# Kernel tuning notes

Hardware: AMD Instinct MI355X
Metric: run time of the kernel (lower is better)

Reference implementation:

```python
import jax, jax.numpy as jnp
import numpy as np

B, T, C, H = 4, 2048, 2048, 16
HD = C // H  # head_size = 128
EPS = 1e-5


def layernorm(x, g, b):
    mu = jnp.mean(x, axis=-1, keepdims=True)
    var = jnp.var(x, axis=-1, keepdims=True)
    return (x - mu) * jax.lax.rsqrt(var + EPS) * g + b


def setup_inputs() -> dict:
    key = jax.random.key(0)
    ks = jax.random.split(key, 12)
    s_attn = 1.0 / np.sqrt(C)
    s_ffn1 = 1.0 / np.sqrt(C)
    s_ffn2 = 1.0 / np.sqrt(4 * C)
    return {
        "x": jax.random.normal(ks[0], (B, T, C), jnp.float32),
        "Wq": jax.random.normal(ks[1], (H, C, HD), jnp.float32) * s_attn,
        "Wk": jax.random.normal(ks[2], (H, C, HD), jnp.float32) * s_attn,
        "Wv": jax.random.normal(ks[3], (H, C, HD), jnp.float32) * s_attn,
        "Wp": jax.random.normal(ks[4], (C, C), jnp.float32) * s_attn,
        "bp": jnp.zeros((C,), jnp.float32),
        "W1": jax.random.normal(ks[5], (C, 4 * C), jnp.float32) * s_ffn1,
        "b1": jnp.zeros((4 * C,), jnp.float32),
        "W2": jax.random.normal(ks[6], (4 * C, C), jnp.float32) * s_ffn2,
        "b2": jnp.zeros((C,), jnp.float32),
        "g1": jnp.ones((C,), jnp.float32),
        "beta1": jnp.zeros((C,), jnp.float32),
        "g2": jnp.ones((C,), jnp.float32),
        "beta2": jnp.zeros((C,), jnp.float32),
    }


def reference(x, Wq, Wk, Wv, Wp, bp, W1, b1, W2, b2, g1, beta1, g2, beta2):
    # --- attention sublayer (pre-LN, causal) ---
    h = layernorm(x, g1, beta1)
    q = jnp.einsum("btc,hcd->bhtd", h, Wq)
    k = jnp.einsum("bsc,hcd->bhsd", h, Wk)
    v = jnp.einsum("bsc,hcd->bhsd", h, Wv)
    scores = jnp.einsum("bhtd,bhsd->bhts", q, k) / jnp.sqrt(jnp.asarray(HD, x.dtype))
    causal = jnp.tril(jnp.ones((T, T), bool))
    scores = jnp.where(causal, scores, jnp.asarray(-jnp.inf, x.dtype))
    w = jax.nn.softmax(scores, axis=-1)  # dropout = identity (eval mode)
    o = jnp.einsum("bhts,bhsd->bhtd", w, v)
    o = o.transpose(0, 2, 1, 3).reshape(B, T, C)  # concat heads
    x = x + o @ Wp + bp
    # --- feed-forward sublayer ---
    h2 = layernorm(x, g2, beta2)
    f = jax.nn.gelu(h2 @ W1 + b1, approximate=False)
    x = x + f @ W2 + b2
    return x
```

## Files before the change

### kernel.cpp

```cpp
#include <hip/hip_runtime.h>
#include <math.h>

#define B_ 4
#define T_ 2048
#define C_ 2048
#define H_ 16
#define HD_ 128

typedef __attribute__((ext_vector_type(8))) short short8;
typedef __attribute__((ext_vector_type(4))) float f32x4;
typedef unsigned short u16;

__device__ __forceinline__ u16 f2bf(float f) {
  union { float f; unsigned u; } v; v.f = f;
  unsigned r = v.u + 0x7FFFu + ((v.u >> 16) & 1u);
  return (u16)(r >> 16);
}

__device__ __forceinline__ void gld16(const void* g, void* l) {
  __builtin_amdgcn_global_load_lds(
      (__attribute__((address_space(1))) void*)(void*)g,
      (__attribute__((address_space(3))) void*)l, 16, 0, 0);
}

__global__ __launch_bounds__(256) void tconv(const float* __restrict__ in,
                                             u16* __restrict__ out,
                                             int K, int N,
                                             long inBS, long outBS) {
  __shared__ float tile[32][33];
  const float* inb = in + (long)blockIdx.z * inBS;
  u16* outb = out + (long)blockIdx.z * outBS;
  int k0 = blockIdx.x << 5, n0 = blockIdx.y << 5;
  int t = threadIdx.x;
  {
    int kk = t >> 3, nn = (t & 7) << 2;
    float4 v = *(const float4*)(inb + (long)(k0 + kk) * N + n0 + nn);
    tile[kk][nn + 0] = v.x; tile[kk][nn + 1] = v.y;
    tile[kk][nn + 2] = v.z; tile[kk][nn + 3] = v.w;
  }
  __syncthreads();
  {
    int nn = t >> 3, kk = (t & 7) << 2;
    ushort4 o;
    o.x = f2bf(tile[kk + 0][nn]); o.y = f2bf(tile[kk + 1][nn]);
    o.z = f2bf(tile[kk + 2][nn]); o.w = f2bf(tile[kk + 3][nn]);
    *(ushort4*)(outb + (long)(n0 + nn) * K + k0 + kk) = o;
  }
}

__global__ __launch_bounds__(256) void ln_rows(const float* __restrict__ x,
                                               const float* __restrict__ gam,
                                               const float* __restrict__ bet,
                                               u16* __restrict__ out) {
  int row = blockIdx.x;
  const float* xr = x + (size_t)row * C_;
  int t = threadIdx.x;
  float4 v0 = *(const float4*)(xr + t * 8);
  float4 v1 = *(const float4*)(xr + t * 8 + 4);
  float s = v0.x + v0.y + v0.z + v0.w + v1.x + v1.y + v1.z + v1.w;
  float ss = v0.x * v0.x + v0.y * v0.y + v0.z * v0.z + v0.w * v0.w +
             v1.x * v1.x + v1.y * v1.y + v1.z * v1.z + v1.w * v1.w;
  for (int d = 32; d > 0; d >>= 1) {
    s += __shfl_down(s, d);
    ss += __shfl_down(ss, d);
  }
  __shared__ float red[8];
  int wv = t >> 6;
  if ((t & 63) == 0) { red[wv] = s; red[4 + wv] = ss; }
  __syncthreads();
  s = red[0] + red[1] + red[2] + red[3];
  ss = red[4] + red[5] + red[6] + red[7];
  float mu = s * (1.0f / C_);
  float var = ss * (1.0f / C_) - mu * mu;
  float rs = rsqrtf(var + 1e-5f);
  int c = t * 8;
  float vv[8] = {v0.x, v0.y, v0.z, v0.w, v1.x, v1.y, v1.z, v1.w};
  ushort4 o0, o1;
  o0.x = f2bf((vv[0] - mu) * rs * gam[c + 0] + bet[c + 0]);
  o0.y = f2bf((vv[1] - mu) * rs * gam[c + 1] + bet[c + 1]);
  o0.z = f2bf((vv[2] - mu) * rs * gam[c + 2] + bet[c + 2]);
  o0.w = f2bf((vv[3] - mu) * rs * gam[c + 3] + bet[c + 3]);
  o1.x = f2bf((vv[4] - mu) * rs * gam[c + 4] + bet[c + 4]);
  o1.y = f2bf((vv[5] - mu) * rs * gam[c + 5] + bet[c + 5]);
  o1.z = f2bf((vv[6] - mu) * rs * gam[c + 6] + bet[c + 6]);
  o1.w = f2bf((vv[7] - mu) * rs * gam[c + 7] + bet[c + 7]);
  *(ushort4*)(out + (size_t)row * C_ + c) = o0;
  *(ushort4*)(out + (size_t)row * C_ + c + 4) = o1;
}

template <int EPI>
__global__ __launch_bounds__(512, 2) void gemm256(
    const u16* __restrict__ A, const u16* __restrict__ BT,
    int M, int N, int K, int lda, int ldb,
    u16* __restrict__ oq, u16* __restrict__ ok, u16* __restrict__ ovt,
    float* __restrict__ of32, const float* __restrict__ resid,
    const float* __restrict__ bias, u16* __restrict__ obf, int addBias) {
  extern __shared__ char smem[];
  int nbx = N >> 8;
  int nwg = gridDim.x;
  int flat = blockIdx.x;
  int sw = (flat & 7) * (nwg >> 3) + (flat >> 3);
  int bx = sw % nbx, by = sw / nbx;
  int m0 = by << 8, n0 = bx << 8;
  int tid = threadIdx.x;
  int lane = tid & 63, wave = tid >> 6;
  int wm = wave >> 2, wn = wave & 3;
  int l15 = lane & 15, l16 = lane >> 4;
  int nt = K >> 6;

  f32x4 acc[8][4] = {};
  short8 af[4][2], bf[4][2];

  auto stage = [&](int b, int r, int k0) {
    int row = (r & 3) * 64 + (tid >> 3);
    int lslot = (tid & 7) ^ (row & 7);
    char* dst = smem + ((r < 4) ? 0 : 65536) + b * 32768 + (r & 3) * 8192 + tid * 16;
    const u16* src = ((r < 4) ? (A + (long)(m0 + row) * lda)
                              : (BT + (long)(n0 + row) * ldb)) +
                     k0 + lslot * 8;
    gld16(src, dst);
  };
  auto ldA = [&](int cur, int mf, int kk) {
    int row = wm * 128 + mf * 16 + l15;
    int slot = (kk * 4 + l16) ^ (row & 7);
    return *(const short8*)(smem + cur * 32768 + row * 128 + slot * 16);
  };
  auto ldB = [&](int cur, int nf, int kk) {
    int row = wn * 64 + nf * 16 + l15;
    int slot = (kk * 4 + l16) ^ (row & 7);
    return *(const short8*)(smem + 65536 + cur * 32768 + row * 128 + slot * 16);
  };

#pragma unroll
  for (int r = 0; r < 8; ++r) stage(0, r, 0);

  for (int t = 0; t < nt; ++t) {
    int cur = t & 1, nxt = cur ^ 1;
    bool more = (t + 1) < nt;
    int k1 = (t + 1) << 6;
    if (more) {
      stage(nxt, 0, k1); stage(nxt, 1, k1); stage(nxt, 2, k1);
      asm volatile("s_waitcnt vmcnt(3)" ::: "memory");
    } else {
      asm volatile("s_waitcnt vmcnt(0)" ::: "memory");
    }
    __builtin_amdgcn_s_barrier();
#pragma unroll
    for (int mq = 0; mq < 4; ++mq)
#pragma unroll
      for (int kk = 0; kk < 2; ++kk) af[mq][kk] = ldA(cur, mq, kk);
#pragma unroll
    for (int nq = 0; nq < 2; ++nq)
#pragma unroll
      for (int kk = 0; kk < 2; ++kk) bf[nq][kk] = ldB(cur, nq, kk);
    if (more) { stage(nxt, 3, k1); stage(nxt, 4, k1); stage(nxt, 5, k1); }
    __builtin_amdgcn_s_barrier();
    asm volatile("s_waitcnt lgkmcnt(0)" ::: "memory");
    __builtin_amdgcn_s_setprio(1);
#pragma unroll
    for (int mq = 0; mq < 4; ++mq)
#pragma unroll
      for (int nq = 0; nq < 2; ++nq)
#pragma unroll
        for (int kk = 0; kk < 2; ++kk)
          acc[mq][nq] = __builtin_amdgcn_mfma_f32_16x16x32_bf16(
              af[mq][kk], bf[nq][kk], acc[mq][nq], 0, 0, 0);
    __builtin_amdgcn_s_setprio(0);
    __builtin_amdgcn_s_barrier();
#pragma unroll
    for (int nq = 2; nq < 4; ++nq)
#pragma unroll
      for (int kk = 0; kk < 2; ++kk) bf[nq][kk] = ldB(cur, nq, kk);
    if (more) { stage(nxt, 6, k1); stage(nxt, 7, k1); }
    __builtin_amdgcn_s_barrier();
    asm volatile("s_waitcnt lgkmcnt(0)" ::: "memory");
    __builtin_amdgcn_s_setprio(1);
#pragma unroll
    for (int mq = 0; mq < 4; ++mq)
#pragma unroll
      for (int nq = 2; nq < 4; ++nq)
#pragma unroll
        for (int kk = 0; kk < 2; ++kk)
          acc[mq][nq] = __builtin_amdgcn_mfma_f32_16x16x32_bf16(
              af[mq][kk], bf[nq][kk], acc[mq][nq], 0, 0, 0);
    __builtin_amdgcn_s_setprio(0);
    __builtin_amdgcn_s_barrier();
#pragma unroll
    for (int mq = 0; mq < 4; ++mq)
#pragma unroll
      for (int kk = 0; kk < 2; ++kk) af[mq][kk] = ldA(cur, 4 + mq, kk);
    __builtin_amdgcn_s_barrier();
    asm volatile("s_waitcnt lgkmcnt(0)" ::: "memory");
    __builtin_amdgcn_s_setprio(1);
#pragma unroll
    for (int mq = 0; mq < 4; ++mq)
#pragma unroll
      for (int nq = 0; nq < 2; ++nq)
#pragma unroll
        for (int kk = 0; kk < 2; ++kk)
          acc[4 + mq][nq] = __builtin_amdgcn_mfma_f32_16x16x32_bf16(
              af[mq][kk], bf[nq][kk], acc[4 + mq][nq], 0, 0, 0);
    __builtin_amdgcn_s_setprio(0);
    __builtin_amdgcn_s_barrier();
    __builtin_amdgcn_s_setprio(1);
#pragma unroll
    for (int mq = 0; mq < 4; ++mq)
#pragma unroll
      for (int nq = 2; nq < 4; ++nq)
#pragma unroll
        for (int kk = 0; kk < 2; ++kk)
          acc[4 + mq][nq] = __builtin_amdgcn_mfma_f32_16x16x32_bf16(
              af[mq][kk], bf[nq][kk], acc[4 + mq][nq], 0, 0, 0);
    __builtin_amdgcn_s_setprio(0);
    __builtin_amdgcn_s_barrier();
  }

#pragma unroll
  for (int mf = 0; mf < 8; ++mf) {
#pragma unroll
    for (int nf = 0; nf < 4; ++nf) {
      int rowf = m0 + wm * 128 + mf * 16 + l16 * 4;
      int col = n0 + wn * 64 + nf * 16 + l15;
      if constexpr (EPI == 0) {
        int seg = col >> 11, cn = col & 2047;
        int hh = cn >> 7, dd = cn & 127;
        int bb = rowf >> 11, t0 = rowf & 2047;
        if (seg == 2) {
          ushort4 o;
          o.x = f2bf(acc[mf][nf][0]); o.y = f2bf(acc[mf][nf][1]);
          o.z = f2bf(acc[mf][nf][2]); o.w = f2bf(acc[mf][nf][3]);
          *(ushort4*)(ovt + ((long)(bb * H_ + hh) * HD_ + dd) * T_ + t0) = o;
        } else {
          u16* dst = (seg == 0) ? oq : ok;
#pragma unroll
          for (int r = 0; r < 4; ++r)
            dst[((long)(bb * H_ + hh) * T_ + t0 + r) * HD_ + dd] =
                f2bf(acc[mf][nf][r]);
        }
      } else if constexpr (EPI == 1) {
#pragma unroll
        for (int r = 0; r < 4; ++r) {
          long idx = (long)(rowf + r) * N + col;
          of32[idx] = resid[idx] + bias[col] + acc[mf][nf][r];
        }
      } else if constexpr (EPI == 2) {
#pragma unroll
        for (int r = 0; r < 4; ++r) {
          float v = acc[mf][nf][r] + bias[col];
          float g = 0.5f * v * (1.0f + erff(v * 0.70710678118654752f));
          obf[(long)(rowf + r) * N + col] = f2bf(g);
        }
      } else {
#pragma unroll
        for (int r = 0; r < 4; ++r) {
          long idx = (long)(rowf + r) * N + col;
          float v = acc[mf][nf][r];
          if (addBias) v += bias[col];
          of32[idx] += v;
        }
      }
    }
  }
}

__global__ __launch_bounds__(256) void attn_fwd(const u16* __restrict__ q,
                                                const u16* __restrict__ k,
                                                const u16* __restrict__ vt,
                                                u16* __restrict__ o) {
  __shared__ u16 Ks[64 * 128];
  __shared__ u16 Vs[128 * 64];
  __shared__ u16 Ps[4][32 * 64];
  int bid = blockIdx.x;
  int bh = bid & 63;
  int qb = 15 - (bid >> 6);
  int q0 = qb << 7;
  int tid = threadIdx.x, lane = tid & 63, wave = tid >> 6;
  int l15 = lane & 15, l16 = lane >> 4;
  int wq0 = q0 + wave * 32;

  short8 qf[2][4];
#pragma unroll
  for (int rf = 0; rf < 2; ++rf)
#pragma unroll
    for (int kk = 0; kk < 4; ++kk)
      qf[rf][kk] = *(const short8*)(q + ((long)bh * T_ + wq0 + rf * 16 + l15) * HD_ +
                                    kk * 32 + l16 * 8);

  f32x4 accO[2][8] = {};
  float m_r[2][4], l_r[2][4];
#pragma unroll
  for (int rf = 0; rf < 2; ++rf)
#pragma unroll
    for (int r = 0; r < 4; ++r) { m_r[rf][r] = -INFINITY; l_r[rf][r] = 0.f; }
  const float sc = 0.08838834764831845f * 1.4426950408889634f;

  int nt = (q0 >> 6) + 2;
  int off0 = wave * 4096 + lane * 16;

  int4 kreg[4], vreg[4];
  auto regload = [&](int t) {
    int s0 = t << 6;
#pragma unroll
    for (int it = 0; it < 4; ++it) {
      int off = off0 + it * 1024;
      int krow = off >> 8;
      kreg[it] = *(const int4*)((const char*)(k + ((long)bh * T_ + s0 + krow) * HD_) +
                                (off & 255));
      int dd = off >> 7;
      vreg[it] = *(const int4*)((const char*)(vt + ((long)bh * HD_ + dd) * T_ + s0) +
                                (off & 127));
    }
  };
  auto dswrite = [&]() {
#pragma unroll
    for (int it = 0; it < 4; ++it) {
      int off = off0 + it * 1024;
      int krow = off >> 8;
      *(int4*)((char*)Ks + (off ^ ((krow & 7) << 4))) = kreg[it];
      int dd = off >> 7;
      *(int4*)((char*)Vs + (off ^ ((dd & 7) << 4))) = vreg[it];
    }
  };

  regload(0);
  dswrite();
  __syncthreads();

  for (int t = 0; t < nt; ++t) {
    int s0 = t << 6;
    bool more = (t + 1 < nt);
    if (more) regload(t + 1);

    if (s0 <= wq0 + 31) {
      bool needmask = (s0 + 63 > wq0);
#pragma unroll
      for (int rf = 0; rf < 2; ++rf) {
        f32x4 S[4];
#pragma unroll
        for (int sb = 0; sb < 4; ++sb) {
          f32x4 s = {};
#pragma unroll
          for (int kk = 0; kk < 4; ++kk) {
            int srow = sb * 16 + l15;
            int kb = srow * 256 + (((kk * 4 + l16) ^ (srow & 7)) << 4);
            short8 kf = *(const short8*)((const char*)Ks + kb);
            s = __builtin_amdgcn_mfma_f32_16x16x32_bf16(qf[rf][kk], kf, s, 0, 0, 0);
          }
          S[sb] = s;
        }
        float mxl[4];
        bool growL = false;
#pragma unroll
        for (int r = 0; r < 4; ++r) {
          int tt = wq0 + rf * 16 + 4 * l16 + r;
          float mx = -INFINITY;
#pragma unroll
          for (int sb = 0; sb < 4; ++sb) {
            float v = S[sb][r] * sc;
            if (needmask && (s0 + sb * 16 + l15 > tt)) v = -INFINITY;
            S[sb][r] = v;
            mx = fmaxf(mx, v);
          }
          mxl[r] = mx;
          growL = growL || (mx > m_r[rf][r] + 8.0f);
        }
        bool anyg = __any(growL);
        float al[4];
        if (anyg) {
#pragma unroll
          for (int r = 0; r < 4; ++r) {
            float mx = mxl[r];
            mx = fmaxf(mx, __shfl_xor(mx, 1));
            mx = fmaxf(mx, __shfl_xor(mx, 2));
            mx = fmaxf(mx, __shfl_xor(mx, 4));
            mx = fmaxf(mx, __shfl_xor(mx, 8));
            float mo = m_r[rf][r];
            float mn = fmaxf(mo, mx);
            al[r] = exp2f(mo - mn);
            m_r[rf][r] = mn;
          }
        } else {
#pragma unroll
          for (int r = 0; r < 4; ++r) al[r] = 1.0f;
        }
#pragma unroll
        for (int r = 0; r < 4; ++r) {
          float mn = m_r[rf][r];
          int prow = rf * 16 + 4 * l16 + r;
          float rs = 0.f;
#pragma unroll
          for (int sb = 0; sb < 4; ++sb) {
            float p = exp2f(S[sb][r] - mn);
            rs += p;
            int pb = (prow * 128 + (sb * 16 + l15) * 2) ^ ((prow & 7) << 4);
            *(u16*)((char*)Ps[wave] + pb) = f2bf(p);
          }
          rs += __shfl_xor(rs, 1);
          rs += __shfl_xor(rs, 2);
          rs += __shfl_xor(rs, 4);
          rs += __shfl_xor(rs, 8);
          l_r[rf][r] = l_r[rf][r] * al[r] + rs;
        }
        if (anyg) {
#pragma unroll
          for (int db = 0; db < 8; ++db)
#pragma unroll
            for (int r = 0; r < 4; ++r) accO[rf][db][r] *= al[r];
        }
        short8 pf[2];
#pragma unroll
        for (int st = 0; st < 2; ++st) {
          int prow = rf * 16 + l15;
          int pb = (prow * 128 + (st * 4 + l16) * 16) ^ ((prow & 7) << 4);
          pf[st] = *(const short8*)((const char*)Ps[wave] + pb);
        }
#pragma unroll
        for (int db = 0; db < 8; ++db) {
#pragma unroll
          for (int st = 0; st < 2; ++st) {
            int vrow = db * 16 + l15;
            int vb = (vrow * 128 + (st * 4 + l16) * 16) ^ ((vrow & 7) << 4);
            short8 vf = *(const short8*)((const char*)Vs + vb);
            accO[rf][db] = __builtin_amdgcn_mfma_f32_16x16x32_bf16(pf[st], vf,
                                                                   accO[rf][db], 0, 0, 0);
          }
        }
      }
    }
    __syncthreads();
    if (more) {
      dswrite();
      __syncthreads();
    }
  }

  int bb = bh >> 4, hh = bh & 15;
#pragma unroll
  for (int rf = 0; rf < 2; ++rf) {
    float inv[4];
#pragma unroll
    for (int r = 0; r < 4; ++r) inv[r] = 1.0f / l_r[rf][r];
#pragma unroll
    for (int db = 0; db < 8; ++db)
#pragma unroll
      for (int r = 0; r < 4; ++r) {
        int tt = wq0 + rf * 16 + 4 * l16 + r;
        o[((long)bb * T_ + tt) * C_ + hh * HD_ + db * 16 + l15] =
            f2bf(accO[rf][db][r] * inv[r]);
      }
  }
}

extern "C" void kernel_launch(void* const* d_in, const int* in_sizes, int n_in,
                              void* d_out, int out_size, void* d_ws, size_t ws_size,
                              hipStream_t stream) {
  (void)in_sizes; (void)n_in; (void)out_size; (void)ws_size;
  const float* x   = (const float*)d_in[0];
  const float* Wq  = (const float*)d_in[1];
  const float* Wk  = (const float*)d_in[2];
  const float* Wv  = (const float*)d_in[3];
  const float* Wp  = (const float*)d_in[4];
  const float* bp  = (const float*)d_in[5];
  const float* W1  = (const float*)d_in[6];
  const float* b1  = (const float*)d_in[7];
  const float* W2  = (const float*)d_in[8];
  const float* b2  = (const float*)d_in[9];
  const float* g1  = (const float*)d_in[10];
  const float* be1 = (const float*)d_in[11];
  const float* g2  = (const float*)d_in[12];
  const float* be2 = (const float*)d_in[13];
  float* out = (float*)d_out;

  (void)hipFuncSetAttribute((const void*)gemm256<0>,
                            hipFuncAttributeMaxDynamicSharedMemorySize, 131072);
  (void)hipFuncSetAttribute((const void*)gemm256<1>,
                            hipFuncAttributeMaxDynamicSharedMemorySize, 131072);
  (void)hipFuncSetAttribute((const void*)gemm256<2>,
                            hipFuncAttributeMaxDynamicSharedMemorySize, 131072);
  (void)hipFuncSetAttribute((const void*)gemm256<3>,
                            hipFuncAttributeMaxDynamicSharedMemorySize, 131072);

  char* ws = (char*)d_ws;
  size_t off = 0;
  auto alloc = [&](size_t n) {
    void* p = ws + off;
    off += (n + 255) & ~(size_t)255;
    return p;
  };
  u16* wqkvT = (u16*)alloc((size_t)6144 * 2048 * 2);
  u16* wpT   = (u16*)alloc((size_t)2048 * 2048 * 2);
  u16* w1T   = (u16*)alloc((size_t)8192 * 2048 * 2);
  u16* w2T   = (u16*)alloc((size_t)2048 * 8192 * 2);
  u16* hb    = (u16*)alloc((size_t)8192 * 2048 * 2);
  u16* qbuf  = (u16*)alloc((size_t)8192 * 2048 * 2);
  u16* kbuf  = (u16*)alloc((size_t)8192 * 2048 * 2);
  u16* vtbuf = (u16*)alloc((size_t)8192 * 2048 * 2);
  u16* ob = hb;
  u16* fb = qbuf;

  tconv<<<dim3(64, 4, 16), 256, 0, stream>>>(Wq, wqkvT, 2048, 128,
                                             (long)2048 * 128, (long)128 * 2048);
  tconv<<<dim3(64, 4, 16), 256, 0, stream>>>(Wk, wqkvT + (size_t)2048 * 2048, 2048, 128,
                                             (long)2048 * 128, (long)128 * 2048);
  tconv<<<dim3(64, 4, 16), 256, 0, stream>>>(Wv, wqkvT + (size_t)4096 * 2048, 2048, 128,
                                             (long)2048 * 128, (long)128 * 2048);
  tconv<<<dim3(64, 64, 1), 256, 0, stream>>>(Wp, wpT, 2048, 2048, 0, 0);
  tconv<<<dim3(64, 256, 1), 256, 0, stream>>>(W1, w1T, 2048, 8192, 0, 0);
  tconv<<<dim3(256, 64, 1), 256, 0, stream>>>(W2, w2T, 8192, 2048, 0, 0);

  ln_rows<<<8192, 256, 0, stream>>>(x, g1, be1, hb);
  gemm256<0><<<768, 512, 131072, stream>>>(hb, wqkvT, 8192, 6144, 2048, 2048, 2048,
                                           qbuf, kbuf, vtbuf, nullptr, nullptr,
                                           nullptr, nullptr, 0);
  attn_fwd<<<1024, 256, 0, stream>>>(qbuf, kbuf, vtbuf, ob);
  gemm256<1><<<256, 512, 131072, stream>>>(ob, wpT, 8192, 2048, 2048, 2048, 2048,
                                           nullptr, nullptr, nullptr, out, x, bp,
                                           nullptr, 0);

  ln_rows<<<8192, 256, 0, stream>>>(out, g2, be2, hb);
  for (int c = 0; c < 2; ++c) {
    gemm256<2><<<512, 512, 131072, stream>>>(hb, w1T + (size_t)c * 4096 * 2048,
                                             8192, 4096, 2048, 2048, 2048,
                                             nullptr, nullptr, nullptr, nullptr,
                                             nullptr, b1 + c * 4096, fb, 0);
    gemm256<3><<<256, 512, 131072, stream>>>(fb, w2T + (size_t)c * 4096,
                                             8192, 2048, 4096, 4096, 8192,
                                             nullptr, nullptr, nullptr, out,
                                             nullptr, b2, nullptr, c == 0 ? 1 : 0);
  }
}
```

Before: 1.350 ms.

## Compute transposed S tile and pass P to PV MFMA via lane shuffles instead of LDS

Swaps the MFMA operands for QK^T so each lane holds one query's scores. Row max and row sum then need only two cross-lane shuffles, with one scalar m/l per lane instead of four. The softmax probabilities are packed to bf16 with v_cvt_pk_bf16_f32 and rearranged into the PV A-operand layout with ds_bpermute shuffles, which removes the per-wave Ps LDS staging buffer. Less LDS per block allows a launch-bounds hint of 3 blocks per CU, at the cost of more shuffle instructions and register pressure.

New measurement: 1.411 ms. +4.5%, slower.

```diff
diff --git a/kernel.cpp b/kernel.cpp
--- a/kernel.cpp
+++ b/kernel.cpp
@@ -10,6 +10,7 @@
 typedef __attribute__((ext_vector_type(8))) short short8;
 typedef __attribute__((ext_vector_type(4))) float f32x4;
 typedef unsigned short u16;
+typedef unsigned int u32;
 
 __device__ __forceinline__ u16 f2bf(float f) {
   union { float f; unsigned u; } v; v.f = f;
@@ -263,13 +264,12 @@
   }
 }
 
-__global__ __launch_bounds__(256) void attn_fwd(const u16* __restrict__ q,
-                                                const u16* __restrict__ k,
-                                                const u16* __restrict__ vt,
-                                                u16* __restrict__ o) {
+__global__ __launch_bounds__(256, 3) void attn_fwd(const u16* __restrict__ q,
+                                                   const u16* __restrict__ k,
+                                                   const u16* __restrict__ vt,
+                                                   u16* __restrict__ o) {
   __shared__ u16 Ks[64 * 128];
   __shared__ u16 Vs[128 * 64];
-  __shared__ u16 Ps[4][32 * 64];
   int bid = blockIdx.x;
   int bh = bid & 63;
   int qb = 15 - (bid >> 6);
@@ -287,11 +287,8 @@
                                     kk * 32 + l16 * 8);
 
   f32x4 accO[2][8] = {};
-  float m_r[2][4], l_r[2][4];
-#pragma unroll
-  for (int rf = 0; rf < 2; ++rf)
-#pragma unroll
-    for (int r = 0; r < 4; ++r) { m_r[rf][r] = -INFINITY; l_r[rf][r] = 0.f; }
+  float m_r[2] = {-INFINITY, -INFINITY};
+  float l_r[2] = {0.f, 0.f};
   const float sc = 0.08838834764831845f * 1.4426950408889634f;
 
   int nt = (q0 >> 6) + 2;
@@ -344,75 +341,75 @@
             int srow = sb * 16 + l15;
             int kb = srow * 256 + (((kk * 4 + l16) ^ (srow & 7)) << 4);
             short8 kf = *(const short8*)((const char*)Ks + kb);
-            s = __builtin_amdgcn_mfma_f32_16x16x32_bf16(qf[rf][kk], kf, s, 0, 0, 0);
+            s = __builtin_amdgcn_mfma_f32_16x16x32_bf16(kf, qf[rf][kk], s, 0, 0, 0);
           }
           S[sb] = s;
         }
-        float mxl[4];
-        bool growL = false;
-#pragma unroll
-        for (int r = 0; r < 4; ++r) {
-          int tt = wq0 + rf * 16 + 4 * l16 + r;
-          float mx = -INFINITY;
-#pragma unroll
-          for (int sb = 0; sb < 4; ++sb) {
+        int qabs = wq0 + rf * 16 + l15;
+        float mx = -INFINITY;
+#pragma unroll
+        for (int sb = 0; sb < 4; ++sb)
+#pragma unroll
+          for (int r = 0; r < 4; ++r) {
             float v = S[sb][r] * sc;
-            if (needmask && (s0 + sb * 16 + l15 > tt)) v = -INFINITY;
+            if (needmask && (s0 + sb * 16 + 4 * l16 + r > qabs)) v = -INFINITY;
             S[sb][r] = v;
             mx = fmaxf(mx, v);
           }
-          mxl[r] = mx;
-          growL = growL || (mx > m_r[rf][r] + 8.0f);
-        }
-        bool anyg = __any(growL);
-        float al[4];
+        mx = fmaxf(mx, __shfl_xor(mx, 16));
+        mx = fmaxf(mx, __shfl_xor(mx, 32));
+        bool grow = mx > m_r[rf] + 8.0f;
+        bool anyg = __any(grow);
+        float al = 1.0f;
         if (anyg) {
-#pragma unroll
-          for (int r = 0; r < 4; ++r) {
-            float mx = mxl[r];
-            mx = fmaxf(mx, __shfl_xor(mx, 1));
-            mx = fmaxf(mx, __shfl_xor(mx, 2));
-            mx = fmaxf(mx, __shfl_xor(mx, 4));
-            mx = fmaxf(mx, __shfl_xor(mx, 8));
-            float mo = m_r[rf][r];
-            float mn = fmaxf(mo, mx);
-            al[r] = exp2f(mo - mn);
-            m_r[rf][r] = mn;
-          }
-        } else {
-#pragma unroll
-          for (int r = 0; r < 4; ++r) al[r] = 1.0f;
-        }
-#pragma unroll
-        for (int r = 0; r < 4; ++r) {
-          float mn = m_r[rf][r];
-          int prow = rf * 16 + 4 * l16 + r;
-          float rs = 0.f;
-#pragma unroll
-          for (int sb = 0; sb < 4; ++sb) {
-            float p = exp2f(S[sb][r] - mn);
-            rs += p;
-            int pb = (prow * 128 + (sb * 16 + l15) * 2) ^ ((prow & 7) << 4);
-            *(u16*)((char*)Ps[wave] + pb) = f2bf(p);
-          }
-          rs += __shfl_xor(rs, 1);
-          rs += __shfl_xor(rs, 2);
-          rs += __shfl_xor(rs, 4);
-          rs += __shfl_xor(rs, 8);
-          l_r[rf][r] = l_r[rf][r] * al[r] + rs;
-        }
+          float mn = fmaxf(m_r[rf], mx);
+          al = exp2f(m_r[rf] - mn);
+          m_r[rf] = mn;
+        }
+        float mcur = m_r[rf];
+        u32 dw[4][2];
+        float rs = 0.f;
+#pragma unroll
+        for (int sb = 0; sb < 4; ++sb) {
+          float p0 = exp2f(S[sb][0] - mcur), p1 = exp2f(S[sb][1] - mcur);
+          float p2 = exp2f(S[sb][2] - mcur), p3 = exp2f(S[sb][3] - mcur);
+          rs += (p0 + p1) + (p2 + p3);
+          asm("v_cvt_pk_bf16_f32 %0, %1, %2" : "=v"(dw[sb][0]) : "v"(p0), "v"(p1));
+          asm("v_cvt_pk_bf16_f32 %0, %1, %2" : "=v"(dw[sb][1]) : "v"(p2), "v"(p3));
+        }
+        rs += __shfl_xor(rs, 16);
+        rs += __shfl_xor(rs, 32);
+        l_r[rf] = l_r[rf] * al + rs;
         if (anyg) {
+          float alr[4];
+#pragma unroll
+          for (int r = 0; r < 4; ++r)
+            alr[r] = __shfl(al, (lane & 48) | (4 * l16 + r));
 #pragma unroll
           for (int db = 0; db < 8; ++db)
 #pragma unroll
-            for (int r = 0; r < 4; ++r) accO[rf][db][r] *= al[r];
-        }
-        short8 pf[2];
+            for (int r = 0; r < 4; ++r) accO[rf][db][r] *= alr[r];
+        }
+        int srcA = ((lane & 16) << 1) | l15;
+        int srcB = srcA + 16;
+        bool hig = (lane & 32) != 0;
+        short8 pa[2];
 #pragma unroll
         for (int st = 0; st < 2; ++st) {
-          int prow = rf * 16 + l15;
-          int pb = (prow * 128 + (st * 4 + l16) * 16) ^ ((prow & 7) << 4);
-          pf[st] = *(const short8*)((const char*)Ps[wave] + pb);
+          u32 t00 = __shfl((int)dw[2 * st][0], srcA);
+          u32 t10 = __shfl((int)dw[2 * st + 1][0], srcA);
+          u32 t01 = __shfl((int)dw[2 * st][1], srcA);
+          u32 t11 = __shfl((int)dw[2 * st + 1][1], srcA);
+          u32 u00 = __shfl((int)dw[2 * st][0], srcB);
+          u32 u10 = __shfl((int)dw[2 * st + 1][0], srcB);
+          u32 u01 = __shfl((int)dw[2 * st][1], srcB);
+          u32 u11 = __shfl((int)dw[2 * st + 1][1], srcB);
+          union { u32 d[4]; short8 s; } pu;
+          pu.d[0] = hig ? t10 : t00;
+          pu.d[1] = hig ? t11 : t01;
+          pu.d[2] = hig ? u10 : u00;
+          pu.d[3] = hig ? u11 : u01;
+          pa[st] = pu.s;
         }
 #pragma unroll
         for (int db = 0; db < 8; ++db) {
@@ -421,7 +418,7 @@
             int vrow = db * 16 + l15;
             int vb = (vrow * 128 + (st * 4 + l16) * 16) ^ ((vrow & 7) << 4);
             short8 vf = *(const short8*)((const char*)Vs + vb);
-            accO[rf][db] = __builtin_amdgcn_mfma_f32_16x16x32_bf16(pf[st], vf,
+            accO[rf][db] = __builtin_amdgcn_mfma_f32_16x16x32_bf16(pa[st], vf,
                                                                    accO[rf][db], 0, 0, 0);
           }
         }
@@ -437,9 +434,11 @@
   int bb = bh >> 4, hh = bh & 15;
 #pragma unroll
   for (int rf = 0; rf < 2; ++rf) {
+    float invq = 1.0f / l_r[rf];
     float inv[4];
 #pragma unroll
-    for (int r = 0; r < 4; ++r) inv[r] = 1.0f / l_r[rf][r];
+    for (int r = 0; r < 4; ++r)
+      inv[r] = __shfl(invq, (lane & 48) | (4 * l16 + r));
 #pragma unroll
     for (int db = 0; db < 8; ++db)
 #pragma unroll
```

## Load attention K/V fragments directly from global memory instead of LDS staging

Applied to the files above, without the earlier changes.

Removes the shared-memory staging of K and V tiles, along with the register prefetch and the block-wide barriers, from the attention kernel. Each wave now reads its MFMA K and V fragments straight from global memory, relying on L1/L2 to serve the reuse across the four waves. This also lets each wave skip fully masked tiles on its own, with no barrier coupling. The trade is more global and cache traffic and exposed load latency, since there is no longer any software prefetch.

Result: slower. 1.460 ms (+8.1%).

```diff
diff --git a/kernel.cpp b/kernel.cpp
--- a/kernel.cpp
+++ b/kernel.cpp
@@ -10,6 +10,7 @@
 typedef __attribute__((ext_vector_type(8))) short short8;
 typedef __attribute__((ext_vector_type(4))) float f32x4;
 typedef unsigned short u16;
+typedef unsigned int u32;
 
 __device__ __forceinline__ u16 f2bf(float f) {
   union { float f; unsigned u; } v; v.f = f;
@@ -267,8 +268,6 @@
                                                 const u16* __restrict__ k,
                                                 const u16* __restrict__ vt,
                                                 u16* __restrict__ o) {
-  __shared__ u16 Ks[64 * 128];
-  __shared__ u16 Vs[128 * 64];
   __shared__ u16 Ps[4][32 * 64];
   int bid = blockIdx.x;
   int bh = bid & 63;
@@ -278,6 +277,9 @@
   int l15 = lane & 15, l16 = lane >> 4;
   int wq0 = q0 + wave * 32;
 
+  const u16* kbase = k + (long)bh * T_ * HD_;
+  const u16* vbase = vt + (long)bh * HD_ * T_;
+
   short8 qf[2][4];
 #pragma unroll
   for (int rf = 0; rf < 2; ++rf)
@@ -295,142 +297,101 @@
   const float sc = 0.08838834764831845f * 1.4426950408889634f;
 
   int nt = (q0 >> 6) + 2;
-  int off0 = wave * 4096 + lane * 16;
-
-  int4 kreg[4], vreg[4];
-  auto regload = [&](int t) {
-    int s0 = t << 6;
-#pragma unroll
-    for (int it = 0; it < 4; ++it) {
-      int off = off0 + it * 1024;
-      int krow = off >> 8;
-      kreg[it] = *(const int4*)((const char*)(k + ((long)bh * T_ + s0 + krow) * HD_) +
-                                (off & 255));
-      int dd = off >> 7;
-      vreg[it] = *(const int4*)((const char*)(vt + ((long)bh * HD_ + dd) * T_ + s0) +
-                                (off & 127));
-    }
-  };
-  auto dswrite = [&]() {
-#pragma unroll
-    for (int it = 0; it < 4; ++it) {
-      int off = off0 + it * 1024;
-      int krow = off >> 8;
-      *(int4*)((char*)Ks + (off ^ ((krow & 7) << 4))) = kreg[it];
-      int dd = off >> 7;
-      *(int4*)((char*)Vs + (off ^ ((dd & 7) << 4))) = vreg[it];
-    }
-  };
-
-  regload(0);
-  dswrite();
-  __syncthreads();
 
   for (int t = 0; t < nt; ++t) {
     int s0 = t << 6;
-    bool more = (t + 1 < nt);
-    if (more) regload(t + 1);
-
-    if (s0 <= wq0 + 31) {
-      bool needmask = (s0 + 63 > wq0);
-#pragma unroll
-      for (int rf = 0; rf < 2; ++rf) {
-        f32x4 S[4];
+    if (s0 > wq0 + 31) continue;
+    bool needmask = (s0 + 63 > wq0);
+#pragma unroll
+    for (int rf = 0; rf < 2; ++rf) {
+      f32x4 S[4];
+#pragma unroll
+      for (int sb = 0; sb < 4; ++sb) {
+        f32x4 s = {};
+#pragma unroll
+        for (int kk = 0; kk < 4; ++kk) {
+          short8 kf = *(const short8*)(kbase + (long)(s0 + sb * 16 + l15) * HD_ +
+                                       kk * 32 + l16 * 8);
+          s = __builtin_amdgcn_mfma_f32_16x16x32_bf16(qf[rf][kk], kf, s, 0, 0, 0);
+        }
+        S[sb] = s;
+      }
+      float mxl[4];
+      bool growL = false;
+#pragma unroll
+      for (int r = 0; r < 4; ++r) {
+        int tt = wq0 + rf * 16 + 4 * l16 + r;
+        float mx = -INFINITY;
 #pragma unroll
         for (int sb = 0; sb < 4; ++sb) {
-          f32x4 s = {};
-#pragma unroll
-          for (int kk = 0; kk < 4; ++kk) {
-            int srow = sb * 16 + l15;
-            int kb = srow * 256 + (((kk * 4 + l16) ^ (srow & 7)) << 4);
-            short8 kf = *(const short8*)((const char*)Ks + kb);
-            s = __builtin_amdgcn_mfma_f32_16x16x32_bf16(qf[rf][kk], kf, s, 0, 0, 0);
-          }
-          S[sb] = s;
-        }
-        float mxl[4];
-        bool growL = false;
+          float v = S[sb][r] * sc;
+          if (needmask && (s0 + sb * 16 + l15 > tt)) v = -INFINITY;
+          S[sb][r] = v;
+          mx = fmaxf(mx, v);
+        }
+        mxl[r] = mx;
+        growL = growL || (mx > m_r[rf][r] + 8.0f);
+      }
+      bool anyg = __any(growL);
+      float al[4];
+      if (anyg) {
 #pragma unroll
         for (int r = 0; r < 4; ++r) {
-          int tt = wq0 + rf * 16 + 4 * l16 + r;
-          float mx = -INFINITY;
-#pragma unroll
-          for (int sb = 0; sb < 4; ++sb) {
-            float v = S[sb][r] * sc;
-            if (needmask && (s0 + sb * 16 + l15 > tt)) v = -INFINITY;
-            S[sb][r] = v;
-            mx = fmaxf(mx, v);
-          }
-          mxl[r] = mx;
-          growL = growL || (mx > m_r[rf][r] + 8.0f);
-        }
-        bool anyg = __any(growL);
-        float al[4];
-        if (anyg) {
-#pragma unroll
-          for (int r = 0; r < 4; ++r) {
-            float mx = mxl[r];
-            mx = fmaxf(mx, __shfl_xor(mx, 1));
-            mx = fmaxf(mx, __shfl_xor(mx, 2));
-            mx = fmaxf(mx, __shfl_xor(mx, 4));
-            mx = fmaxf(mx, __shfl_xor(mx, 8));
-            float mo = m_r[rf][r];
-            float mn = fmaxf(mo, mx);
-            al[r] = exp2f(mo - mn);
-            m_r[rf][r] = mn;
-          }
-        } else {
-#pragma unroll
-          for (int r = 0; r < 4; ++r) al[r] = 1.0f;
-        }
-#pragma unroll
-        for (int r = 0; r < 4; ++r) {
-          float mn = m_r[rf][r];
-          int prow = rf * 16 + 4 * l16 + r;
-          float rs = 0.f;
-#pragma unroll
-          for (int sb = 0; sb < 4; ++sb) {
-            float p = exp2f(S[sb][r] - mn);
-            rs += p;
-            int pb = (prow * 128 + (sb * 16 + l15) * 2) ^ ((prow & 7) << 4);
-            *(u16*)((char*)Ps[wave] + pb) = f2bf(p);
-          }
-          rs += __shfl_xor(rs, 1);
-          rs += __shfl_xor(rs, 2);
-          rs += __shfl_xor(rs, 4);
-          rs += __shfl_xor(rs, 8);
-          l_r[rf][r] = l_r[rf][r] * al[r] + rs;
-        }
-        if (anyg) {
-#pragma unroll
-          for (int db = 0; db < 8; ++db)
-#pragma unroll
-            for (int r = 0; r < 4; ++r) accO[rf][db][r] *= al[r];
-        }
-        short8 pf[2];
+          float mx = mxl[r];
+          mx = fmaxf(mx, __shfl_xor(mx, 1));
+          mx = fmaxf(mx, __shfl_xor(mx, 2));
+          mx = fmaxf(mx, __shfl_xor(mx, 4));
+          mx = fmaxf(mx, __shfl_xor(mx, 8));
+          float mo = m_r[rf][r];
+          float mn = fmaxf(mo, mx);
+          al[r] = exp2f(mo - mn);
+          m_r[rf][r] = mn;
+        }
+      } else {
+#pragma unroll
+        for (int r = 0; r < 4; ++r) al[r] = 1.0f;
+      }
+#pragma unroll
+      for (int r = 0; r < 4; ++r) {
+        float mn = m_r[rf][r];
+        int prow = rf * 16 + 4 * l16 + r;
+        float rs = 0.f;
+#pragma unroll
+        for (int sb = 0; sb < 4; ++sb) {
+          float p = exp2f(S[sb][r] - mn);
+          rs += p;
+          int pb = (prow * 128 + (sb * 16 + l15) * 2) ^ ((prow & 7) << 4);
+          *(u16*)((char*)Ps[wave] + pb) = f2bf(p);
+        }
+        rs += __shfl_xor(rs, 1);
+        rs += __shfl_xor(rs, 2);
+        rs += __shfl_xor(rs, 4);
+        rs += __shfl_xor(rs, 8);
+        l_r[rf][r] = l_r[rf][r] * al[r] + rs;
+      }
+      if (anyg) {
+#pragma unroll
+        for (int db = 0; db < 8; ++db)
+#pragma unroll
+          for (int r = 0; r < 4; ++r) accO[rf][db][r] *= al[r];
+      }
+      short8 pf[2];
+#pragma unroll
+      for (int st = 0; st < 2; ++st) {
+        int prow = rf * 16 + l15;
+        int pb = (prow * 128 + (st * 4 + l16) * 16) ^ ((prow & 7) << 4);
+        pf[st] = *(const short8*)((const char*)Ps[wave] + pb);
+      }
+#pragma unroll
+      for (int db = 0; db < 8; ++db) {
 #pragma unroll
         for (int st = 0; st < 2; ++st) {
-          int prow = rf * 16 + l15;
-          int pb = (prow * 128 + (st * 4 + l16) * 16) ^ ((prow & 7) << 4);
-          pf[st] = *(const short8*)((const char*)Ps[wave] + pb);
-        }
-#pragma unroll
-        for (int db = 0; db < 8; ++db) {
-#pragma unroll
-          for (int st = 0; st < 2; ++st) {
-            int vrow = db * 16 + l15;
-            int vb = (vrow * 128 + (st * 4 + l16) * 16) ^ ((vrow & 7) << 4);
-            short8 vf = *(const short8*)((const char*)Vs + vb);
-            accO[rf][db] = __builtin_amdgcn_mfma_f32_16x16x32_bf16(pf[st], vf,
-                                                                   accO[rf][db], 0, 0, 0);
-          }
-        }
-      }
-    }
-    __syncthreads();
-    if (more) {
-      dswrite();
-      __syncthreads();
+          short8 vf = *(const short8*)(vbase + (long)(db * 16 + l15) * T_ +
+                                       s0 + (st * 4 + l16) * 8);
+          accO[rf][db] = __builtin_amdgcn_mfma_f32_16x16x32_bf16(pf[st], vf,
+                                                                 accO[rf][db], 0, 0, 0);
+        }
+      }
     }
   }
 
```

## Halve attention query tile to 64 rows, one 16-row fragment per wave

Applied to the files above, without the earlier changes.

The attention kernel now gives each block 64 query rows instead of 128, so each wave handles 16 rows instead of 32. The grid doubles to 2048 blocks, and the P scratch buffer and per-wave register state (Q fragments, accumulators, softmax stats) shrink by half. The aim is more parallelism and occupancy, plus finer causal load balancing with less masked work on diagonal tiles. The cost is that each K/V tile loaded into shared memory is reused by half as many query rows, which roughly doubles total K/V traffic and synchronisation per unit of work.

Result: faster. 1.313 ms (-2.8%).

```diff
diff --git a/kernel.cpp b/kernel.cpp
--- a/kernel.cpp
+++ b/kernel.cpp
@@ -10,6 +10,7 @@
 typedef __attribute__((ext_vector_type(8))) short short8;
 typedef __attribute__((ext_vector_type(4))) float f32x4;
 typedef unsigned short u16;
+typedef unsigned int u32;
 
 __device__ __forceinline__ u16 f2bf(float f) {
   union { float f; unsigned u; } v; v.f = f;
@@ -269,32 +270,28 @@
                                                 u16* __restrict__ o) {
   __shared__ u16 Ks[64 * 128];
   __shared__ u16 Vs[128 * 64];
-  __shared__ u16 Ps[4][32 * 64];
+  __shared__ u16 Ps[4][16 * 64];
   int bid = blockIdx.x;
   int bh = bid & 63;
-  int qb = 15 - (bid >> 6);
-  int q0 = qb << 7;
+  int qb = 31 - (bid >> 6);
+  int q0 = qb << 6;
   int tid = threadIdx.x, lane = tid & 63, wave = tid >> 6;
   int l15 = lane & 15, l16 = lane >> 4;
-  int wq0 = q0 + wave * 32;
-
-  short8 qf[2][4];
-#pragma unroll
-  for (int rf = 0; rf < 2; ++rf)
-#pragma unroll
-    for (int kk = 0; kk < 4; ++kk)
-      qf[rf][kk] = *(const short8*)(q + ((long)bh * T_ + wq0 + rf * 16 + l15) * HD_ +
-                                    kk * 32 + l16 * 8);
-
-  f32x4 accO[2][8] = {};
-  float m_r[2][4], l_r[2][4];
-#pragma unroll
-  for (int rf = 0; rf < 2; ++rf)
-#pragma unroll
-    for (int r = 0; r < 4; ++r) { m_r[rf][r] = -INFINITY; l_r[rf][r] = 0.f; }
+  int wq0 = q0 + wave * 16;
+
+  short8 qf[4];
+#pragma unroll
+  for (int kk = 0; kk < 4; ++kk)
+    qf[kk] = *(const short8*)(q + ((long)bh * T_ + wq0 + l15) * HD_ +
+                              kk * 32 + l16 * 8);
+
+  f32x4 accO[8] = {};
+  float m_r[4], l_r[4];
+#pragma unroll
+  for (int r = 0; r < 4; ++r) { m_r[r] = -INFINITY; l_r[r] = 0.f; }
   const float sc = 0.08838834764831845f * 1.4426950408889634f;
 
-  int nt = (q0 >> 6) + 2;
+  int nt = qb + 1;
   int off0 = wave * 4096 + lane * 16;
 
   int4 kreg[4], vreg[4];
@@ -331,99 +328,96 @@
     bool more = (t + 1 < nt);
     if (more) regload(t + 1);
 
-    if (s0 <= wq0 + 31) {
+    if (s0 <= wq0 + 15) {
       bool needmask = (s0 + 63 > wq0);
-#pragma unroll
-      for (int rf = 0; rf < 2; ++rf) {
-        f32x4 S[4];
+      f32x4 S[4];
+#pragma unroll
+      for (int sb = 0; sb < 4; ++sb) {
+        f32x4 s = {};
+#pragma unroll
+        for (int kk = 0; kk < 4; ++kk) {
+          int srow = sb * 16 + l15;
+          int kb = srow * 256 + (((kk * 4 + l16) ^ (srow & 7)) << 4);
+          short8 kf = *(const short8*)((const char*)Ks + kb);
+          s = __builtin_amdgcn_mfma_f32_16x16x32_bf16(qf[kk], kf, s, 0, 0, 0);
+        }
+        S[sb] = s;
+      }
+      float mxl[4];
+      bool growL = false;
+#pragma unroll
+      for (int r = 0; r < 4; ++r) {
+        int tt = wq0 + 4 * l16 + r;
+        float mx = -INFINITY;
 #pragma unroll
         for (int sb = 0; sb < 4; ++sb) {
-          f32x4 s = {};
-#pragma unroll
-          for (int kk = 0; kk < 4; ++kk) {
-            int srow = sb * 16 + l15;
-            int kb = srow * 256 + (((kk * 4 + l16) ^ (srow & 7)) << 4);
-            short8 kf = *(const short8*)((const char*)Ks + kb);
-            s = __builtin_amdgcn_mfma_f32_16x16x32_bf16(qf[rf][kk], kf, s, 0, 0, 0);
-          }
-          S[sb] = s;
-        }
-        float mxl[4];
-        bool growL = false;
+          float v = S[sb][r] * sc;
+          if (needmask && (s0 + sb * 16 + l15 > tt)) v = -INFINITY;
+          S[sb][r] = v;
+          mx = fmaxf(mx, v);
+        }
+        mxl[r] = mx;
+        growL = growL || (mx > m_r[r] + 8.0f);
+      }
+      bool anyg = __any(growL);
+      float al[4];
+      if (anyg) {
 #pragma unroll
         for (int r = 0; r < 4; ++r) {
-          int tt = wq0 + rf * 16 + 4 * l16 + r;
-          float mx = -INFINITY;
-#pragma unroll
-          for (int sb = 0; sb < 4; ++sb) {
-            float v = S[sb][r] * sc;
-            if (needmask && (s0 + sb * 16 + l15 > tt)) v = -INFINITY;
-            S[sb][r] = v;
-            mx = fmaxf(mx, v);
-          }
-          mxl[r] = mx;
-          growL = growL || (mx > m_r[rf][r] + 8.0f);
-        }
-        bool anyg = __any(growL);
-        float al[4];
-        if (anyg) {
-#pragma unroll
-          for (int r = 0; r < 4; ++r) {
-            float mx = mxl[r];
-            mx = fmaxf(mx, __shfl_xor(mx, 1));
-            mx = fmaxf(mx, __shfl_xor(mx, 2));
-            mx = fmaxf(mx, __shfl_xor(mx, 4));
-            mx = fmaxf(mx, __shfl_xor(mx, 8));
-            float mo = m_r[rf][r];
-            float mn = fmaxf(mo, mx);
-            al[r] = exp2f(mo - mn);
-            m_r[rf][r] = mn;
-          }
-        } else {
-#pragma unroll
-          for (int r = 0; r < 4; ++r) al[r] = 1.0f;
-        }
-#pragma unroll
-        for (int r = 0; r < 4; ++r) {
-          float mn = m_r[rf][r];
-          int prow = rf * 16 + 4 * l16 + r;
-          float rs = 0.f;
-#pragma unroll
-          for (int sb = 0; sb < 4; ++sb) {
-            float p = exp2f(S[sb][r] - mn);
-            rs += p;
-            int pb = (prow * 128 + (sb * 16 + l15) * 2) ^ ((prow & 7) << 4);
-            *(u16*)((char*)Ps[wave] + pb) = f2bf(p);
-          }
-          rs += __shfl_xor(rs, 1);
-          rs += __shfl_xor(rs, 2);
-          rs += __shfl_xor(rs, 4);
-          rs += __shfl_xor(rs, 8);
-          l_r[rf][r] = l_r[rf][r] * al[r] + rs;
-        }
-        if (anyg) {
-#pragma unroll
-          for (int db = 0; db < 8; ++db)
-#pragma unroll
-            for (int r = 0; r < 4; ++r) accO[rf][db][r] *= al[r];
-        }
-        short8 pf[2];
+          float mx = mxl[r];
+          mx = fmaxf(mx, __shfl_xor(mx, 1));
+          mx = fmaxf(mx, __shfl_xor(mx, 2));
+          mx = fmaxf(mx, __shfl_xor(mx, 4));
+          mx = fmaxf(mx, __shfl_xor(mx, 8));
+          float mo = m_r[r];
+          float mn = fmaxf(mo, mx);
+          al[r] = exp2f(mo - mn);
+          m_r[r] = mn;
+        }
+      } else {
+#pragma unroll
+        for (int r = 0; r < 4; ++r) al[r] = 1.0f;
+      }
+#pragma unroll
+      for (int r = 0; r < 4; ++r) {
+        float mn = m_r[r];
+        int prow = 4 * l16 + r;
+        float rs = 0.f;
+#pragma unroll
+        for (int sb = 0; sb < 4; ++sb) {
+          float p = exp2f(S[sb][r] - mn);
+          rs += p;
+          int pb = (prow * 128 + (sb * 16 + l15) * 2) ^ ((prow & 7) << 4);
+          *(u16*)((char*)Ps[wave] + pb) = f2bf(p);
+        }
+        rs += __shfl_xor(rs, 1);
+        rs += __shfl_xor(rs, 2);
+        rs += __shfl_xor(rs, 4);
+        rs += __shfl_xor(rs, 8);
+        l_r[r] = l_r[r] * al[r] + rs;
+      }
+      if (anyg) {
+#pragma unroll
+        for (int db = 0; db < 8; ++db)
+#pragma unroll
+          for (int r = 0; r < 4; ++r) accO[db][r] *= al[r];
+      }
+      short8 pf[2];
+#pragma unroll
+      for (int st = 0; st < 2; ++st) {
+        int prow = l15;
+        int pb = (prow * 128 + (st * 4 + l16) * 16) ^ ((prow & 7) << 4);
+        pf[st] = *(const short8*)((const char*)Ps[wave] + pb);
+      }
+#pragma unroll
+      for (int db = 0; db < 8; ++db) {
 #pragma unroll
         for (int st = 0; st < 2; ++st) {
-          int prow = rf * 16 + l15;
-          int pb = (prow * 128 + (st * 4 + l16) * 16) ^ ((prow & 7) << 4);
-          pf[st] = *(const short8*)((const char*)Ps[wave] + pb);
-        }
-#pragma unroll
-        for (int db = 0; db < 8; ++db) {
-#pragma unroll
-          for (int st = 0; st < 2; ++st) {
-            int vrow = db * 16 + l15;
-            int vb = (vrow * 128 + (st * 4 + l16) * 16) ^ ((vrow & 7) << 4);
-            short8 vf = *(const short8*)((const char*)Vs + vb);
-            accO[rf][db] = __builtin_amdgcn_mfma_f32_16x16x32_bf16(pf[st], vf,
-                                                                   accO[rf][db], 0, 0, 0);
-          }
+          int vrow = db * 16 + l15;
+          int vb = (vrow * 128 + (st * 4 + l16) * 16) ^ ((vrow & 7) << 4);
+          short8 vf = *(const short8*)((const char*)Vs + vb);
+          accO[db] = __builtin_amdgcn_mfma_f32_16x16x32_bf16(pf[st], vf,
+                                                             accO[db], 0, 0, 0);
         }
       }
     }
@@ -435,20 +429,17 @@
   }
 
   int bb = bh >> 4, hh = bh & 15;
-#pragma unroll
-  for (int rf = 0; rf < 2; ++rf) {
-    float inv[4];
-#pragma unroll
-    for (int r = 0; r < 4; ++r) inv[r] = 1.0f / l_r[rf][r];
-#pragma unroll
-    for (int db = 0; db < 8; ++db)
-#pragma unroll
-      for (int r = 0; r < 4; ++r) {
-        int tt = wq0 + rf * 16 + 4 * l16 + r;
-        o[((long)bb * T_ + tt) * C_ + hh * HD_ + db * 16 + l15] =
-            f2bf(accO[rf][db][r] * inv[r]);
-      }
-  }
+  float inv[4];
+#pragma unroll
+  for (int r = 0; r < 4; ++r) inv[r] = 1.0f / l_r[r];
+#pragma unroll
+  for (int db = 0; db < 8; ++db)
+#pragma unroll
+    for (int r = 0; r < 4; ++r) {
+      int tt = wq0 + 4 * l16 + r;
+      o[((long)bb * T_ + tt) * C_ + hh * HD_ + db * 16 + l15] =
+          f2bf(accO[db][r] * inv[r]);
+    }
 }
 
 extern "C" void kernel_launch(void* const* d_in, const int* in_sizes, int n_in,
@@ -512,7 +503,7 @@
   gemm256<0><<<768, 512, 131072, stream>>>(hb, wqkvT, 8192, 6144, 2048, 2048, 2048,
                                            qbuf, kbuf, vtbuf, nullptr, nullptr,
                                            nullptr, nullptr, 0);
-  attn_fwd<<<1024, 256, 0, stream>>>(qbuf, kbuf, vtbuf, ob);
+  attn_fwd<<<2048, 256, 0, stream>>>(qbuf, kbuf, vtbuf, ob);
   gemm256<1><<<256, 512, 131072, stream>>>(ob, wpT, 8192, 2048, 2048, 2048, 2048,
                                            nullptr, nullptr, nullptr, out, x, bp,
                                            nullptr, 0);
```
